# Optimization experiments

Measured on AMD Instinct MI355X. Metric: run time of the kernel, lower is better.

The kernel has to match this reference:

```python
import jax, jax.numpy as jnp
import numpy as np

EPS = 1e-6
SINKHORN_ITERS = 8
TEMPERATURE = 1.0
B, N, D = 4, 8192, 512
E, OUT = 8, 512
H = 1


def setup_inputs() -> dict:
    key = jax.random.key(0)
    k1, k2, k3 = jax.random.split(key, 3)
    x = jax.random.normal(k1, (B, N, D), dtype=jnp.float32)
    gate_weight = jax.random.normal(k2, (H, D, E), dtype=jnp.float32)
    experts = jax.random.normal(k3, (E, D, OUT), dtype=jnp.float32) * 0.02
    return {"x": x, "gate_weight": gate_weight, "experts": experts}


def _sinkhorn(logits):
    # logits: (b, h, n, e). log(clamp(.,eps)) then alternating row/col log-normalization.
    t = jnp.log(jnp.clip(logits, EPS)) / TEMPERATURE
    for _ in range(SINKHORN_ITERS):
        t = t - jax.nn.logsumexp(t, axis=-2, keepdims=True)  # normalize over tokens n
        t = t - jax.nn.logsumexp(t, axis=-1, keepdims=True)  # normalize over experts e
    return jnp.exp(t)


def reference(x, gate_weight, experts):
    b, n, d = x.shape
    e = experts.shape[0]
    m = n // e  # tokens per expert
    xh = x[:, None, :, :]  # b 1 n d  (single-headed -> h=1)
    gate_logits = jnp.einsum('bhnd,hde->bhne', xh, gate_weight)
    gates = _sinkhorn(gate_logits)  # b h n e
    # topk over token dim n, per expert: move n to last axis for lax.top_k
    g_t = jnp.swapaxes(gates, -1, -2)  # b h e n
    vals, idx = jax.lax.top_k(g_t, m)  # (b h e m), (b h e m)
    gate_values = jnp.transpose(vals, (2, 0, 1, 3))[..., None]  # e b h m 1
    # gather routed tokens: routed[e,b,h,m,d] = x[b,h,idx[b,h,e,m],d]
    routed = jnp.take_along_axis(xh[:, :, None, :, :], idx[..., None], axis=3)  # b h e m d
    routed = jnp.transpose(routed, (2, 0, 1, 3, 4))  # e b h m d
    expert_w = experts[:, None, :, :]  # e h i o with h=1 (rearrange 'e i o -> e 1 i o')
    outputs = jnp.einsum('ebhmi,ehio->ebhmo', routed, expert_w)  # e b h m o
    outputs = outputs * gate_values
    # scatter back (set semantics, matching einx set_at)
    bh_idx = idx.reshape(b, 1, e * m)  # b h (e m)
    bh_vals = jnp.transpose(outputs, (1, 2, 0, 3, 4)).reshape(b, 1, e * m, outputs.shape[-1])
    def scat(i1, v1):
        return jnp.zeros((n, v1.shape[-1]), dtype=v1.dtype).at[i1].set(v1)
    routed_back = jax.vmap(jax.vmap(scat))(bh_idx, bh_vals)  # b h n o
    return routed_back[:, 0]  # b n o
```

## Files before the change

### kernel.cpp

```cpp
#include <hip/hip_runtime.h>
#include <hip/hip_bf16.h>

#define BB 4
#define NN 8192
#define DD 512
#define EE 8
#define OUTD 512
#define TOPM 1024
#define EPSV 1e-6f
#define ITERS 8

using s16x8 = __attribute__((ext_vector_type(8))) short;
using f32x4 = __attribute__((ext_vector_type(4))) float;
typedef unsigned long long u64;

__device__ __forceinline__ unsigned short f2bf(float f) {
  unsigned u = __float_as_uint(f);
  return (unsigned short)((u + 0x7FFFu + ((u >> 16) & 1u)) >> 16);
}

__device__ __forceinline__ void gll16(const void* g, void* l) {
  __builtin_amdgcn_global_load_lds((const __attribute__((address_space(1))) void*)g,
                                   (__attribute__((address_space(3))) void*)l, 16, 0, 0);
}

__global__ __launch_bounds__(256) void k_gate(const float* __restrict__ x,
                                              const float* __restrict__ gw,
                                              float* __restrict__ t0,
                                              unsigned short* __restrict__ xbf,
                                              int* __restrict__ eo,
                                              int* __restrict__ counts,
                                              const float* __restrict__ W,
                                              unsigned short* __restrict__ WT) {
  const int tid = threadIdx.x;
  if (blockIdx.x >= 2048) {
    __shared__ float tl[32][33];
    const int widx = blockIdx.x - 2048;
    const int e = widx >> 8, rem = widx & 255;
    const int k0 = (rem >> 4) * 32, n0 = (rem & 15) * 32;
    const int ty = tid >> 5, tx = tid & 31;
    const float* src = W + ((long)e * DD + k0) * OUTD + n0;
#pragma unroll
    for (int j = 0; j < 4; ++j)
      tl[ty + j * 8][tx] = src[(long)(ty + j * 8) * OUTD + tx];
    __syncthreads();
    unsigned short* dst = WT + ((long)e * OUTD + n0) * DD + k0;
#pragma unroll
    for (int j = 0; j < 4; ++j)
      dst[(long)(ty + j * 8) * DD + tx] = f2bf(tl[tx][ty + j * 8]);
    return;
  }
  if (tid < 16) eo[blockIdx.x * 16 + tid] = -1;
  if (blockIdx.x == 0 && tid >= 64 && tid < 64 + BB * EE) counts[tid - 64] = 0;
  const int lane = tid & 63;
  const int w    = tid >> 6;
  float gwf[64];
  const float* gb = gw + (lane * 8) * EE;
#pragma unroll
  for (int q = 0; q < 16; ++q) {
    float4 t = *(const float4*)(gb + q * 4);
    gwf[q * 4 + 0] = t.x; gwf[q * 4 + 1] = t.y;
    gwf[q * 4 + 2] = t.z; gwf[q * 4 + 3] = t.w;
  }
#pragma unroll
  for (int q = 0; q < 64; ++q) asm volatile("" : "+v"(gwf[q]));

  const long row0 = (long)blockIdx.x * 16 + w * 4;
  float4 xa[4], xb[4];
#pragma unroll
  for (int i = 0; i < 4; ++i) {
    const float* xr = x + (row0 + i) * DD + lane * 8;
    xa[i] = *(const float4*)(xr);
    xb[i] = *(const float4*)(xr + 4);
  }
  float vout[4];
#pragma unroll
  for (int i = 0; i < 4; ++i) {
    float xv[8] = {xa[i].x, xa[i].y, xa[i].z, xa[i].w,
                   xb[i].x, xb[i].y, xb[i].z, xb[i].w};
    s16x8 xo;
#pragma unroll
    for (int j = 0; j < 8; ++j) xo[j] = (short)f2bf(xv[j]);
    *(s16x8*)(xbf + (row0 + i) * DD + lane * 8) = xo;

    float acc[8] = {0.f,0.f,0.f,0.f,0.f,0.f,0.f,0.f};
#pragma unroll
    for (int q = 0; q < 8; ++q)
#pragma unroll
      for (int e = 0; e < 8; ++e) acc[e] += xv[q] * gwf[q * 8 + e];
    const bool o1 = lane & 1;
    float own, oth, b0, b1, b2, b3, c0, c1, v;
    own = o1 ? acc[1] : acc[0]; oth = o1 ? acc[0] : acc[1];
    b0 = own + __shfl_xor(oth, 1);
    own = o1 ? acc[3] : acc[2]; oth = o1 ? acc[2] : acc[3];
    b1 = own + __shfl_xor(oth, 1);
    own = o1 ? acc[5] : acc[4]; oth = o1 ? acc[4] : acc[5];
    b2 = own + __shfl_xor(oth, 1);
    own = o1 ? acc[7] : acc[6]; oth = o1 ? acc[6] : acc[7];
    b3 = own + __shfl_xor(oth, 1);
    const bool o2 = lane & 2;
    own = o2 ? b1 : b0; oth = o2 ? b0 : b1;
    c0 = own + __shfl_xor(oth, 2);
    own = o2 ? b3 : b2; oth = o2 ? b2 : b3;
    c1 = own + __shfl_xor(oth, 2);
    const bool o4 = lane & 4;
    own = o4 ? c1 : c0; oth = o4 ? c0 : c1;
    v = own + __shfl_xor(oth, 4);
    v += __shfl_xor(v, 8);
    v += __shfl_xor(v, 16);
    v += __shfl_xor(v, 32);
    vout[i] = v;
  }
  const int gsel = lane >> 3;
  float vsel = vout[0];
  vsel = (gsel == 1) ? vout[1] : vsel;
  vsel = (gsel == 2) ? vout[2] : vsel;
  vsel = (gsel == 3) ? vout[3] : vsel;
  if (lane < 32) t0[row0 * EE + lane] = logf(fmaxf(vsel, EPSV));
}

__global__ __launch_bounds__(1024, 4) void k_topk(const float* __restrict__ t0,
                                                  float* __restrict__ R,
                                                  float* __restrict__ C,
                                                  int* __restrict__ expert_of) {
  __shared__ unsigned key[NN];
  __shared__ int hist[256];
  __shared__ int bcast[2];
  __shared__ int wsum[16];
  __shared__ float ws[16][8], Csh[8], Ssh[8];
  const int b = blockIdx.x >> 3, e = blockIdx.x & 7;
  const int tid = threadIdx.x;
  const int wv = tid >> 6, ln = tid & 63;
  const float* tb = t0 + (long)b * NN * EE;

  float E[8][8], u[8], dl[8];
#pragma unroll
  for (int j = 0; j < 8; ++j) {
    const float* p = tb + (long)(j * 1024 + tid) * EE;
    float4 a = *(const float4*)p, b4 = *(const float4*)(p + 4);
    E[j][0] = expf(a.x);  E[j][1] = expf(a.y);
    E[j][2] = expf(a.z);  E[j][3] = expf(a.w);
    E[j][4] = expf(b4.x); E[j][5] = expf(b4.y);
    E[j][6] = expf(b4.z); E[j][7] = expf(b4.w);
    key[j * 1024 + tid] = __float_as_uint(p[e]);
    u[j] = 1.f;
  }
  for (int it = 0; it < ITERS; ++it) {
    float P[8] = {0.f,0.f,0.f,0.f,0.f,0.f,0.f,0.f};
#pragma unroll
    for (int j = 0; j < 8; ++j)
#pragma unroll
      for (int e2 = 0; e2 < 8; ++e2) P[e2] += E[j][e2] * u[j];
#pragma unroll
    for (int d = 1; d <= 4; d <<= 1) {
#pragma unroll
      for (int e2 = 0; e2 < 8; ++e2) {
        float tmp = __shfl_xor(P[e2], d);
        P[e2] += ((ln & d) == (e2 & d)) ? tmp : 0.f;
      }
    }
    float pv = P[0];
#pragma unroll
    for (int e2 = 1; e2 < 8; ++e2) pv = ((ln & 7) == e2) ? P[e2] : pv;
#pragma unroll
    for (int d = 8; d < 64; d <<= 1) pv += __shfl_xor(pv, d);
    if (ln < 8) ws[wv][ln] = pv;
    __syncthreads();
    if (tid < 64) {
      const int q = ln >> 3, e2 = ln & 7;
      float s = ws[q][e2] + ws[q + 8][e2];
#pragma unroll
      for (int d = 8; d < 64; d <<= 1) s += __shfl_xor(s, d);
      if (ln < 8) { Csh[ln] = 1.f / s; Ssh[ln] = s; }
    }
    __syncthreads();
    float vv[8];
#pragma unroll
    for (int e2 = 0; e2 < 8; ++e2) vv[e2] = Csh[e2];
#pragma unroll
    for (int j = 0; j < 8; ++j) {
      float d0 = E[j][0] * vv[0];
#pragma unroll
      for (int e2 = 1; e2 < 8; ++e2) d0 += E[j][e2] * vv[e2];
      dl[j] = d0;
      u[j] = 1.f / d0;
    }
    __syncthreads();
  }
  if (e == 0) {
#pragma unroll
    for (int j = 0; j < 8; ++j) R[(long)b * NN + j * 1024 + tid] = logf(dl[j]);
    if (tid < 8) C[b * EE + tid] = logf(Ssh[tid]);
  }

  if (tid < 256) hist[tid] = 0;
  __syncthreads();
#pragma unroll
  for (int j = 0; j < 8; ++j) {
    const int n = j * 1024 + tid;
    float f = __uint_as_float(key[n]) - logf(dl[j]);
    unsigned uk = __float_as_uint(f);
    uk = (uk & 0x80000000u) ? ~uk : (uk | 0x80000000u);
    key[n] = uk;
    atomicAdd(&hist[uk >> 24], 1);
  }
  __syncthreads();
  unsigned prefix = 0, mask = 0;
  int k = TOPM;
  for (int shift = 24; shift >= 0; shift -= 8) {
    if (tid < 64) {
      const int4 h4 = *(const int4*)&hist[ln * 4];
      const int r3 = h4.w, r2 = h4.z + r3, r1 = h4.y + r2, r0 = h4.x + r1;
      int suf = r0;
#pragma unroll
      for (int d = 1; d < 64; d <<= 1) {
        int o = __shfl_down(suf, d);
        if (ln + d < 64) suf += o;
      }
      const int above = suf - r0;
      const int cum0 = above + r0, cum1 = above + r1;
      const int cum2 = above + r2, cum3 = above + r3;
      if (cum0 >= k && cum1 < k) { bcast[0] = k - cum1; bcast[1] = ln * 4 + 0; }
      if (cum1 >= k && cum2 < k) { bcast[0] = k - cum2; bcast[1] = ln * 4 + 1; }
      if (cum2 >= k && cum3 < k) { bcast[0] = k - cum3; bcast[1] = ln * 4 + 2; }
      if (cum3 >= k && above < k) { bcast[0] = k - above; bcast[1] = ln * 4 + 3; }
    }
    __syncthreads();
    k = bcast[0];
    prefix |= ((unsigned)bcast[1]) << shift;
    mask |= (255u << shift);
    if (shift == 0) break;
    if (tid < 256) hist[tid] = 0;
    __syncthreads();
    const int nsh = shift - 8;
    for (int n = tid; n < NN; n += 1024) {
      unsigned uk = key[n];
      if ((uk & mask) == prefix) atomicAdd(&hist[(uk >> nsh) & 255], 1);
    }
    __syncthreads();
  }
  const unsigned theta = prefix;
  const int need = k;
  const int base = tid * 8;
  int c = 0;
#pragma unroll
  for (int j = 0; j < 8; ++j) if (key[base + j] == theta) ++c;
  int inc = c;
#pragma unroll
  for (int d = 1; d < 64; d <<= 1) {
    int o = __shfl_up(inc, d);
    if (ln >= d) inc += o;
  }
  if (ln == 63) wsum[wv] = inc;
  __syncthreads();
  if (tid == 0) {
    int runv = 0;
    for (int i = 0; i < 16; ++i) { int t2 = wsum[i]; wsum[i] = runv; runv += t2; }
  }
  __syncthreads();
  int run = wsum[wv] + inc - c;
  int* eo = expert_of + b * NN;
  for (int j = 0; j < 8; ++j) {
    int n = base + j;
    unsigned uk = key[n];
    bool sel = false;
    if (uk > theta) sel = true;
    else if (uk == theta) { if (run < need) sel = true; ++run; }
    if (sel) atomicMax(&eo[n], e);
  }
}

__global__ __launch_bounds__(256) void k_post(const int* __restrict__ expert_of,
                                              const float* __restrict__ t0,
                                              const float* __restrict__ R,
                                              const float* __restrict__ C,
                                              int* __restrict__ counts,
                                              int* __restrict__ lists,
                                              float* __restrict__ gvals,
                                              float* __restrict__ out) {
  const int tid = threadIdx.x;
  if (blockIdx.x >= 128) {
    const int row = (blockIdx.x - 128) * 4 + (tid >> 6);
    if (expert_of[row] >= 0) return;
    const int ln = tid & 63;
    float4 z = make_float4(0.f, 0.f, 0.f, 0.f);
    float4* p = (float4*)(out + (long)row * OUTD) + ln;
    p[0] = z; p[64] = z;
    return;
  }
  __shared__ int hist8[8], base8[8];
  if (tid < 8) hist8[tid] = 0;
  __syncthreads();
  const long i = (long)blockIdx.x * 256 + tid;
  const int b = (int)(i >> 13);
  const int e = expert_of[i];
  int lpos = -1;
  if (e >= 0) lpos = atomicAdd(&hist8[e], 1);
  __syncthreads();
  if (tid < 8 && hist8[tid] > 0)
    base8[tid] = atomicAdd(&counts[b * EE + tid], hist8[tid]);
  __syncthreads();
  if (e >= 0) {
    const int n = (int)(i & (NN - 1));
    const int be = b * EE + e;
    const int slot = be * TOPM + base8[e] + lpos;
    lists[slot] = n;
    gvals[slot] = expf(t0[i * EE + e] - C[be] - R[i]);
  }
}

__global__ __launch_bounds__(256) void k_gemm(const unsigned short* __restrict__ xbf,
                                              const unsigned short* __restrict__ WT,
                                              const int* __restrict__ counts,
                                              const int* __restrict__ lists,
                                              const float* __restrict__ gvals,
                                              float* __restrict__ out) {
  const int id = blockIdx.x;
  const int xq = id >> 8;
  const int be = (id >> 3) & 31;
  const int yq = id & 7;
  const int b = be >> 3, e = be & 7;
  const int cnt = counts[be];
  const int r0 = yq * 128;
  if (r0 >= cnt) return;
  const int c0 = xq * 128;

  __shared__ unsigned short As[128 * 64];
  __shared__ unsigned short Bs[128 * 64];
  __shared__ int   rowTok[128];
  __shared__ float rowG[128];

  const int tid = threadIdx.x;
  if (tid < 128) {
    int r = r0 + tid;
    rowTok[tid] = (r < cnt) ? lists[be * TOPM + r] : -1;
    rowG[tid]   = (r < cnt) ? gvals[be * TOPM + r] : 0.f;
  }
  __syncthreads();

  const int w = tid >> 6, l = tid & 63;
  const int rbase = w * 32 + (l >> 3);
  const int sL = l & 7;
  const unsigned short* xb_b = xbf + (long)b * NN * DD;
  const unsigned short* wt_e = WT + (long)e * OUTD * DD;
  int tokc[4]; int sGa[4], sGb[4];
#pragma unroll
  for (int c = 0; c < 4; ++c) {
    int r = rbase + c * 8;
    int tk = rowTok[r]; if (tk < 0) tk = 0;
    tokc[c] = tk;
    sGa[c] = (sL ^ (r & 7)) * 8;
    sGb[c] = sGa[c];
  }

  const int wr = w >> 1, wc = w & 1;
  const int fr = l & 15, fq = l >> 4;
  int aoff[4][2], boff[4][2];
#pragma unroll
  for (int m = 0; m < 4; ++m) {
#pragma unroll
    for (int kk = 0; kk < 2; ++kk) {
      int row = wr * 64 + m * 16 + fr;
      aoff[m][kk] = row * 64 + (((fq + 4 * kk) ^ (row & 7)) * 8);
      int col = wc * 64 + m * 16 + fr;
      boff[m][kk] = col * 64 + (((fq + 4 * kk) ^ (col & 7)) * 8);
    }
  }

  f32x4 acc[4][4] = {};

#define STAGE(kb) {                                                          \
    int ko = (kb) * 64;                                                      \
    _Pragma("unroll")                                                        \
    for (int c = 0; c < 4; ++c) {                                            \
      int r = rbase + c * 8;                                                 \
      gll16(xb_b + (long)tokc[c] * DD + ko + sGa[c],                         \
            As + (w * 32 + c * 8) * 64);                                     \
      gll16(wt_e + (long)(c0 + r) * DD + ko + sGb[c],                        \
            Bs + (w * 32 + c * 8) * 64);                                     \
    }                                                                        \
  }

  STAGE(0);
  for (int kb = 0; kb < 8; ++kb) {
    __syncthreads();
    s16x8 af[4][2], bf_[4][2];
#pragma unroll
    for (int m = 0; m < 4; ++m) {
      af[m][0] = *(const s16x8*)(As + aoff[m][0]);
      af[m][1] = *(const s16x8*)(As + aoff[m][1]);
      bf_[m][0] = *(const s16x8*)(Bs + boff[m][0]);
      bf_[m][1] = *(const s16x8*)(Bs + boff[m][1]);
    }
    __syncthreads();
    if (kb < 7) STAGE(kb + 1);
#pragma unroll
    for (int kk = 0; kk < 2; ++kk)
#pragma unroll
      for (int m = 0; m < 4; ++m)
#pragma unroll
        for (int n = 0; n < 4; ++n)
          acc[m][n] = __builtin_amdgcn_mfma_f32_16x16x32_bf16(af[m][kk], bf_[n][kk], acc[m][n], 0, 0, 0);
  }
#undef STAGE

#pragma unroll
  for (int m = 0; m < 4; ++m) {
    int rbase2 = wr * 64 + m * 16 + fq * 4;
    int tok[4]; float g[4];
#pragma unroll
    for (int j = 0; j < 4; ++j) { tok[j] = rowTok[rbase2 + j]; g[j] = rowG[rbase2 + j]; }
#pragma unroll
    for (int n = 0; n < 4; ++n) {
      int col = c0 + wc * 64 + n * 16 + fr;
#pragma unroll
      for (int j = 0; j < 4; ++j) {
        if (tok[j] >= 0)
          out[((long)b * NN + tok[j]) * OUTD + col] = acc[m][n][j] * g[j];
      }
    }
  }
}

extern "C" void kernel_launch(void* const* d_in, const int* in_sizes, int n_in,
                              void* d_out, int out_size, void* d_ws, size_t ws_size,
                              hipStream_t stream) {
  const float* x  = (const float*)d_in[0];
  const float* gw = (const float*)d_in[1];
  const float* ex = (const float*)d_in[2];
  float* out = (float*)d_out;

  char* wsb = (char*)d_ws;
  float*          t0     = (float*)(wsb);
  unsigned short* xbf    = (unsigned short*)(wsb + (1l << 20));
  unsigned short* WT     = (unsigned short*)(wsb + (33l << 20));
  const long base = 37l << 20;
  float*          R      = (float*)(wsb + base);
  int*            eo     = (int*)  (wsb + base + (128l << 10));
  int*            lists  = (int*)  (wsb + base + (256l << 10));
  float*          gvals  = (float*)(wsb + base + (384l << 10));
  float*          C      = (float*)(wsb + base + (512l << 10));
  int*            counts = (int*)  (wsb + base + (512l << 10) + 1024);

  k_gate<<<2048 + 2048, 256, 0, stream>>>(x, gw, t0, xbf, eo, counts, ex, WT);
  k_topk<<<BB * EE, 1024, 0, stream>>>(t0, R, C, eo);
  k_post<<<128 + (BB * NN) / 4, 256, 0, stream>>>(eo, t0, R, C, counts, lists, gvals, out);
  k_gemm<<<1024, 256, 0, stream>>>(xbf, WT, counts, lists, gvals, out);
}
```

Before: 106.3 us.

## Triple-buffer gathered GEMM with K=32 stages and vmcnt-based waits

Restructures the routed-expert GEMM main loop from a single 64-wide K buffer with two full syncthreads per step into a three-stage ring of 32-wide K tiles. Loads are issued two stages ahead and completion is tracked with explicit s_waitcnt vmcnt plus a single s_barrier per iteration, using a new XOR swizzle suited to the 32-element row stride. The aim is to overlap global gathers with MFMA work and remove one barrier per step, at the cost of twice as many loop iterations and reliance on hand-counted outstanding loads. It also drops the min-blocks hint from the top-k kernel's launch bounds.

```diff
diff --git a/kernel.cpp b/kernel.cpp
--- a/kernel.cpp
+++ b/kernel.cpp
@@ -119,10 +119,10 @@
   if (lane < 32) t0[row0 * EE + lane] = logf(fmaxf(vsel, EPSV));
 }
 
-__global__ __launch_bounds__(1024, 4) void k_topk(const float* __restrict__ t0,
-                                                  float* __restrict__ R,
-                                                  float* __restrict__ C,
-                                                  int* __restrict__ expert_of) {
+__global__ __launch_bounds__(1024) void k_topk(const float* __restrict__ t0,
+                                               float* __restrict__ R,
+                                               float* __restrict__ C,
+                                               int* __restrict__ expert_of) {
   __shared__ unsigned key[NN];
   __shared__ int hist[256];
   __shared__ int bcast[2];
@@ -325,8 +325,8 @@
   if (r0 >= cnt) return;
   const int c0 = xq * 128;
 
-  __shared__ unsigned short As[128 * 64];
-  __shared__ unsigned short Bs[128 * 64];
+  __shared__ unsigned short As[3][128 * 32];
+  __shared__ unsigned short Bs[3][128 * 32];
   __shared__ int   rowTok[128];
   __shared__ float rowG[128];
 
@@ -339,68 +339,63 @@
   __syncthreads();
 
   const int w = tid >> 6, l = tid & 63;
-  const int rbase = w * 32 + (l >> 3);
-  const int sL = l & 7;
   const unsigned short* xb_b = xbf + (long)b * NN * DD;
   const unsigned short* wt_e = WT + (long)e * OUTD * DD;
-  int tokc[4]; int sGa[4], sGb[4];
-#pragma unroll
-  for (int c = 0; c < 4; ++c) {
-    int r = rbase + c * 8;
+  const unsigned short* gA[2];
+  const unsigned short* gB[2];
+#pragma unroll
+  for (int c = 0; c < 2; ++c) {
+    int r = w * 32 + c * 16 + (l >> 2);
+    int cr = (r ^ (r >> 2)) & 3;
     int tk = rowTok[r]; if (tk < 0) tk = 0;
-    tokc[c] = tk;
-    sGa[c] = (sL ^ (r & 7)) * 8;
-    sGb[c] = sGa[c];
+    gA[c] = xb_b + (long)tk * DD + (((l & 3) ^ cr) * 8);
+    gB[c] = wt_e + (long)(c0 + r) * DD + (((l & 3) ^ cr) * 8);
   }
 
   const int wr = w >> 1, wc = w & 1;
   const int fr = l & 15, fq = l >> 4;
-  int aoff[4][2], boff[4][2];
+  int aoff[4], boff[4];
 #pragma unroll
   for (int m = 0; m < 4; ++m) {
-#pragma unroll
-    for (int kk = 0; kk < 2; ++kk) {
-      int row = wr * 64 + m * 16 + fr;
-      aoff[m][kk] = row * 64 + (((fq + 4 * kk) ^ (row & 7)) * 8);
-      int col = wc * 64 + m * 16 + fr;
-      boff[m][kk] = col * 64 + (((fq + 4 * kk) ^ (col & 7)) * 8);
-    }
+    int row = wr * 64 + m * 16 + fr;
+    int cr = (row ^ (row >> 2)) & 3;
+    aoff[m] = row * 32 + ((fq ^ cr) * 8);
+    int col = wc * 64 + m * 16 + fr;
+    int cc = (col ^ (col >> 2)) & 3;
+    boff[m] = col * 32 + ((fq ^ cc) * 8);
   }
 
   f32x4 acc[4][4] = {};
 
-#define STAGE(kb) {                                                          \
-    int ko = (kb) * 64;                                                      \
-    _Pragma("unroll")                                                        \
-    for (int c = 0; c < 4; ++c) {                                            \
-      int r = rbase + c * 8;                                                 \
-      gll16(xb_b + (long)tokc[c] * DD + ko + sGa[c],                         \
-            As + (w * 32 + c * 8) * 64);                                     \
-      gll16(wt_e + (long)(c0 + r) * DD + ko + sGb[c],                        \
-            Bs + (w * 32 + c * 8) * 64);                                     \
-    }                                                                        \
-  }
-
-  STAGE(0);
-  for (int kb = 0; kb < 8; ++kb) {
-    __syncthreads();
-    s16x8 af[4][2], bf_[4][2];
-#pragma unroll
-    for (int m = 0; m < 4; ++m) {
-      af[m][0] = *(const s16x8*)(As + aoff[m][0]);
-      af[m][1] = *(const s16x8*)(As + aoff[m][1]);
-      bf_[m][0] = *(const s16x8*)(Bs + boff[m][0]);
-      bf_[m][1] = *(const s16x8*)(Bs + boff[m][1]);
-    }
-    __syncthreads();
-    if (kb < 7) STAGE(kb + 1);
-#pragma unroll
-    for (int kk = 0; kk < 2; ++kk)
-#pragma unroll
-      for (int m = 0; m < 4; ++m)
-#pragma unroll
-        for (int n = 0; n < 4; ++n)
-          acc[m][n] = __builtin_amdgcn_mfma_f32_16x16x32_bf16(af[m][kk], bf_[n][kk], acc[m][n], 0, 0, 0);
+#define STAGE(kb, p) {                                                       \
+    int ko = (kb) * 32;                                                      \
+    gll16(gA[0] + ko, &As[p][(w * 32 +  0) * 32]);                           \
+    gll16(gA[1] + ko, &As[p][(w * 32 + 16) * 32]);                           \
+    gll16(gB[0] + ko, &Bs[p][(w * 32 +  0) * 32]);                           \
+    gll16(gB[1] + ko, &Bs[p][(w * 32 + 16) * 32]);                           \
+  }
+
+  STAGE(0, 0);
+  STAGE(1, 1);
+  for (int kb = 0; kb < 16; ++kb) {
+    const int p = kb - (kb / 3) * 3;
+    if (kb < 15) asm volatile("s_waitcnt vmcnt(4)" ::: "memory");
+    else         asm volatile("s_waitcnt vmcnt(0)" ::: "memory");
+    __builtin_amdgcn_s_barrier();
+    s16x8 af[4], bf_[4];
+#pragma unroll
+    for (int m = 0; m < 4; ++m) af[m] = *(const s16x8*)(&As[p][0] + aoff[m]);
+#pragma unroll
+    for (int n = 0; n < 4; ++n) bf_[n] = *(const s16x8*)(&Bs[p][0] + boff[n]);
+    if (kb < 14) {
+      const int p2 = (kb + 2) - ((kb + 2) / 3) * 3;
+      STAGE(kb + 2, p2);
+    }
+#pragma unroll
+    for (int m = 0; m < 4; ++m)
+#pragma unroll
+      for (int n = 0; n < 4; ++n)
+        acc[m][n] = __builtin_amdgcn_mfma_f32_16x16x32_bf16(af[m], bf_[n], acc[m][n], 0, 0, 0);
   }
 #undef STAGE
 
```

After: 110.6 us. +4.0%, slower.
